# Performance work log

Measured on AMD Instinct MI355X. Metric: run time of the kernel, lower is better.

## Reference

```python
import jax, jax.numpy as jnp
import numpy as np

B, S, D = 8, 2048, 512

def setup_inputs() -> dict:
    key = jax.random.key(0)
    ks = jax.random.split(key, 9)
    scale = 1.0 / np.sqrt(D)
    return {
        "x": jax.random.normal(ks[0], (B, S, D), dtype=jnp.float32),
        "attention_mask": jax.random.uniform(ks[1], (B, S), dtype=jnp.float32),
        "Wq": jax.random.normal(ks[2], (D, D), dtype=jnp.float32) * scale,
        "bq": jax.random.normal(ks[3], (D,), dtype=jnp.float32) * 0.01,
        "Wk": jax.random.normal(ks[4], (D, D), dtype=jnp.float32) * scale,
        "bk": jax.random.normal(ks[5], (D,), dtype=jnp.float32) * 0.01,
        "Wv": jax.random.normal(ks[6], (D, D), dtype=jnp.float32) * scale,
        "bv": jax.random.normal(ks[7], (D,), dtype=jnp.float32) * 0.01,
    }

def reference(x, attention_mask, Wq, bq, Wk, bk, Wv, bv):
    # Single-head self-attention, full O(S^2) scores as in the original.
    q = jnp.einsum('bsd,df->bsf', x, Wq) + bq  # [B,S,D]
    k = jnp.einsum('bsd,df->bsf', x, Wk) + bk
    v = jnp.einsum('bsd,df->bsf', x, Wv) + bv
    scores = jnp.einsum('bqd,bkd->bqk', q, k) / jnp.sqrt(jnp.float32(D))  # [B,S,S]
    attn = jax.nn.softmax(scores, axis=2)
    weighted = jnp.einsum('bqk,bkd->bqd', attn, v)  # [B,S,D]
    # mask applied multiplicatively to the output, per original code
    return weighted * attention_mask[:, :, None]
```

## Files before the change

kernel.cpp:

```cpp
#include <hip/hip_runtime.h>
#include <math.h>
#include <stdint.h>


typedef _Float16 f16x8 __attribute__((ext_vector_type(8)));
typedef _Float16 f16x4 __attribute__((ext_vector_type(4)));
typedef _Float16 f16x2 __attribute__((ext_vector_type(2)));
typedef float f32x4 __attribute__((ext_vector_type(4)));

__device__ __forceinline__ void async16(const _Float16* g, _Float16* l) {
    __builtin_amdgcn_global_load_lds(
        (const __attribute__((address_space(1))) unsigned int*)(uintptr_t)g,
        (__attribute__((address_space(3))) unsigned int*)(unsigned int)(uintptr_t)l,
        16, 0, 0);
}

__device__ __forceinline__ float frag_sum8(f16x8 v, float acc) {
#if __has_builtin(__builtin_amdgcn_fdot2)
    const f16x2 one2 = {(_Float16)1.f, (_Float16)1.f};
    const f16x2* p = (const f16x2*)&v;
    acc = __builtin_amdgcn_fdot2(p[0], one2, acc, false);
    acc = __builtin_amdgcn_fdot2(p[1], one2, acc, false);
    acc = __builtin_amdgcn_fdot2(p[2], one2, acc, false);
    acc = __builtin_amdgcn_fdot2(p[3], one2, acc, false);
#else
#pragma unroll
    for (int j = 0; j < 8; j++) acc += (float)v[j];
#endif
    return acc;
}

template <bool WITH_RS>
__device__ __forceinline__ void mfma_gemm_core64(
    const _Float16* __restrict__ A, int lda,
    const _Float16* __restrict__ B, int ldb,
    int K, int row0, int col0,
    _Float16* sm, f32x4 acc[4][4], float rs[4])
{
    const int tid  = threadIdx.x;
    const int lane = tid & 63;
    const int wave = tid >> 6;
    const int wm   = wave >> 1, wn = wave & 1;

    const int rc  = lane >> 3;
    const int swz = ((lane & 7) ^ rc) * 8;

    const _Float16* gA[4]; const _Float16* gB[4];
    int lA[4], lB[4];
#pragma unroll
    for (int i = 0; i < 4; i++) {
        int c = wave * 4 + i;
        gA[i] = A + (size_t)(row0 + 8 * c + rc) * lda + swz;
        gB[i] = B + (size_t)(col0 + 8 * c + rc) * ldb + swz;
        lA[i] = c * 512;
        lB[i] = 8192 + c * 512;
    }

    const int fr = lane & 15;
    const int q  = lane >> 4;
    const int fx = fr & 7;

#pragma unroll
    for (int i = 0; i < 4; i++) {
        async16(gA[i], sm + lA[i]);
        async16(gB[i], sm + lB[i]);
    }

    int cur = 0;
    for (int k0 = 0;; k0 += 64) {
        const bool more = (k0 + 64) < K;
        if (more) {
            const int nb = (cur ^ 1) * 16384;
#pragma unroll
            for (int i = 0; i < 4; i++) {
                async16(gA[i] + k0 + 64, sm + nb + lA[i]);
                async16(gB[i] + k0 + 64, sm + nb + lB[i]);
            }
            asm volatile("s_waitcnt vmcnt(8)" ::: "memory");
        } else {
            asm volatile("s_waitcnt vmcnt(0)" ::: "memory");
        }
        __builtin_amdgcn_s_barrier();
        asm volatile("" ::: "memory");

        const _Float16* As = sm + cur * 16384;
        const _Float16* Bs = As + 8192;
#pragma unroll
        for (int step = 0; step < 2; step++) {
            f16x8 af[4], bf[4];
#pragma unroll
            for (int t = 0; t < 4; t++) {
                int ra = wm * 64 + t * 16 + fr;
                int rb = wn * 64 + t * 16 + fr;
                int kc = ((step * 4 + q) ^ fx) * 8;
                af[t] = *(const f16x8*)&As[ra * 64 + kc];
                bf[t] = *(const f16x8*)&Bs[rb * 64 + kc];
            }
            if (WITH_RS) {
#pragma unroll
                for (int t = 0; t < 4; t++) rs[t] = frag_sum8(af[t], rs[t]);
            }
#pragma unroll
            for (int tm = 0; tm < 4; tm++)
#pragma unroll
                for (int tn = 0; tn < 4; tn++)
                    acc[tm][tn] = __builtin_amdgcn_mfma_f32_16x16x32_f16(
                        af[tm], bf[tn], acc[tm][tn], 0, 0, 0);
        }
        asm volatile("" ::: "memory");
        if (!more) break;
        __builtin_amdgcn_s_barrier();
        cur ^= 1;
    }
}

__global__ __launch_bounds__(256) void prep(
    const float* __restrict__ x,
    const float* __restrict__ Wq, const float* __restrict__ Wk,
    const float* __restrict__ Wv,
    _Float16* __restrict__ Xh,
    _Float16* __restrict__ WqT, _Float16* __restrict__ WkT,
    _Float16* __restrict__ WvT)
{
    const int bid = blockIdx.x;
    if (bid < 8192) {
        int i = (bid * 256 + threadIdx.x) * 4;
        float4 v = *(const float4*)(x + i);
        f16x4 h;
        h.x = (_Float16)v.x; h.y = (_Float16)v.y;
        h.z = (_Float16)v.z; h.w = (_Float16)v.w;
        *(f16x4*)&Xh[i] = h;
    } else {
        int t = bid - 8192;
        int z = t >> 10;
        const float* W = (z == 0) ? Wq : (z == 1) ? Wk : Wv;
        _Float16* Wt   = (z == 0) ? WqT : (z == 1) ? WkT : WvT;
        int idx = (t & 1023) * 256 + threadIdx.x;
        int n = idx >> 9, k = idx & 511;
        Wt[idx] = (_Float16)W[k * 512 + n];
    }
}

__global__ __launch_bounds__(256) void proj_mfma(
    const _Float16* __restrict__ Xh,
    const _Float16* __restrict__ WqT, const float* __restrict__ bq,
    const _Float16* __restrict__ WkT, const float* __restrict__ bk,
    const _Float16* __restrict__ WvT, const float* __restrict__ bv,
    _Float16* __restrict__ Qh, _Float16* __restrict__ Kh,
    _Float16* __restrict__ Vt)
{
    __shared__ __align__(16) _Float16 smem[4 * 128 * 64];

    const int z = blockIdx.z;
    f32x4 acc[4][4];
#pragma unroll
    for (int i = 0; i < 4; i++)
#pragma unroll
        for (int j = 0; j < 4; j++) acc[i][j] = (f32x4){0.f, 0.f, 0.f, 0.f};
    float rs_unused[4];

    const int lane = threadIdx.x & 63, wave = threadIdx.x >> 6;
    const int wm = wave >> 1, wn = wave & 1;
    const int er = (lane >> 4) * 4, ec = lane & 15;

    if (z < 2) {
        const _Float16* Wt = (z == 0) ? WqT : WkT;
        const float* bias  = (z == 0) ? bq : bk;
        _Float16* P        = (z == 0) ? Qh : Kh;
        const float sc     = (z == 0) ? 0.04419417382415922f : 1.0f;
        const int row0 = blockIdx.x * 128, col0 = blockIdx.y * 128;
        mfma_gemm_core64<false>(Xh, 512, Wt, 512, 512, row0, col0, smem, acc,
                                rs_unused);
#pragma unroll
        for (int tm = 0; tm < 4; tm++)
#pragma unroll
            for (int tn = 0; tn < 4; tn++) {
                int col = col0 + wn * 64 + tn * 16 + ec;
                float bb = bias[col];
#pragma unroll
                for (int r = 0; r < 4; r++) {
                    int row = row0 + wm * 64 + tm * 16 + er + r;
                    P[(size_t)row * 512 + col] = (_Float16)((acc[tm][tn][r] + bb) * sc);
                }
            }
    } else {
        const int row0 = blockIdx.y * 128;
        const int col0 = blockIdx.x * 128;
        mfma_gemm_core64<false>(WvT, 512, Xh, 512, 512, row0, col0, smem, acc,
                                rs_unused);
#pragma unroll
        for (int tm = 0; tm < 4; tm++)
#pragma unroll
            for (int tn = 0; tn < 4; tn++) {
                int col = col0 + wn * 64 + tn * 16 + ec;
                size_t obase = (size_t)(col >> 11) * (512 * 2048) + (col & 2047);
#pragma unroll
                for (int r = 0; r < 4; r++) {
                    int row = row0 + wm * 64 + tm * 16 + er + r;
                    Vt[obase + (size_t)row * 2048] = (_Float16)(acc[tm][tn][r] + bv[row]);
                }
            }
    }
}

__global__ __launch_bounds__(256) void scores_mfma(
    const _Float16* __restrict__ Qh, const _Float16* __restrict__ Kh,
    _Float16* __restrict__ Sh)
{
    __shared__ __align__(16) _Float16 smem[4 * 128 * 64];
    const int bid = blockIdx.x;
    const int b   = bid & 7;
    const int rem = bid >> 3;
    const int col0 = (rem & 15) * 128;
    const int row0 = (rem >> 4) * 128;

    const _Float16* A = Qh + (size_t)b * 2048 * 512;
    const _Float16* B = Kh + (size_t)b * 2048 * 512;
    _Float16* S = Sh + (size_t)b * 2048 * 2048;

    f32x4 acc[4][4];
#pragma unroll
    for (int i = 0; i < 4; i++)
#pragma unroll
        for (int j = 0; j < 4; j++) acc[i][j] = (f32x4){0.f, 0.f, 0.f, 0.f};
    float rs_unused[4];

    mfma_gemm_core64<false>(A, 512, B, 512, 512, row0, col0, smem, acc,
                            rs_unused);

    const int lane = threadIdx.x & 63, wave = threadIdx.x >> 6;
    const int wm = wave >> 1, wn = wave & 1;
    const int er = (lane >> 4) * 4, ec = lane & 15;
#pragma unroll
    for (int tm = 0; tm < 4; tm++)
#pragma unroll
        for (int tn = 0; tn < 4; tn++) {
            int col = col0 + wn * 64 + tn * 16 + ec;
#pragma unroll
            for (int r = 0; r < 4; r++) {
                int row = row0 + wm * 64 + tm * 16 + er + r;
                S[(size_t)row * 2048 + col] = (_Float16)__expf(acc[tm][tn][r]);
            }
        }
}

__global__ __launch_bounds__(256) void av_mfma(
    const _Float16* __restrict__ Sh, const _Float16* __restrict__ Vt,
    const float* __restrict__ mask, float* __restrict__ out)
{
    __shared__ __align__(16) _Float16 smem[4 * 128 * 64];
    const int bid = blockIdx.x;
    const int b   = bid & 7;
    const int rem = bid >> 3;
    const int col0 = (rem & 3) * 128;
    const int row0 = (rem >> 2) * 128;

    const _Float16* A = Sh + (size_t)b * 2048 * 2048;
    const _Float16* B = Vt + (size_t)b * 512 * 2048;
    float* O = out + (size_t)b * 2048 * 512;
    const float* mk = mask + (size_t)b * 2048;

    f32x4 acc[4][4];
#pragma unroll
    for (int i = 0; i < 4; i++)
#pragma unroll
        for (int j = 0; j < 4; j++) acc[i][j] = (f32x4){0.f, 0.f, 0.f, 0.f};
    float rs[4] = {0.f, 0.f, 0.f, 0.f};

    mfma_gemm_core64<true>(A, 2048, B, 2048, 2048, row0, col0, smem, acc, rs);

    const int lane = threadIdx.x & 63, wave = threadIdx.x >> 6;
    const int wm = wave >> 1, wn = wave & 1;
    const int er = (lane >> 4) * 4, ec = lane & 15;

#pragma unroll
    for (int t = 0; t < 4; t++) {
        rs[t] += __shfl_xor(rs[t], 16, 64);
        rs[t] += __shfl_xor(rs[t], 32, 64);
    }
    __syncthreads();
    float* l_s = (float*)smem;
    if (wn == 0 && lane < 16) {
#pragma unroll
        for (int t = 0; t < 4; t++) l_s[wm * 64 + t * 16 + lane] = rs[t];
    }
    __syncthreads();

#pragma unroll
    for (int tm = 0; tm < 4; tm++)
#pragma unroll
        for (int r = 0; r < 4; r++) {
            int lrow = wm * 64 + tm * 16 + er + r;
            int row = row0 + lrow;
            float s = mk[row] / l_s[lrow];
#pragma unroll
            for (int tn = 0; tn < 4; tn++) {
                int col = col0 + wn * 64 + tn * 16 + ec;
                O[(size_t)row * 512 + col] = acc[tm][tn][r] * s;
            }
        }
}

extern "C" void kernel_launch(void* const* d_in, const int* in_sizes, int n_in,
                              void* d_out, int out_size, void* d_ws, size_t ws_size,
                              hipStream_t stream) {
    const float* x    = (const float*)d_in[0];
    const float* mask = (const float*)d_in[1];
    const float* Wq   = (const float*)d_in[2];
    const float* bq   = (const float*)d_in[3];
    const float* Wk   = (const float*)d_in[4];
    const float* bk   = (const float*)d_in[5];
    const float* Wv   = (const float*)d_in[6];
    const float* bv   = (const float*)d_in[7];
    float* out = (float*)d_out;

    const size_t BSD = (size_t)8 * 2048 * 512;
    _Float16* base = (_Float16*)d_ws;
    _Float16* Qh  = base;
    _Float16* Kh  = Qh + BSD;
    _Float16* Vt  = Kh + BSD;
    _Float16* WqT = Vt + BSD;
    _Float16* WkT = WqT + 512 * 512;
    _Float16* WvT = WkT + 512 * 512;
    _Float16* Xh  = WvT + 512 * 512;
    _Float16* Sh  = Xh;

    dim3 blk(256);
    prep<<<dim3(8192 + 3 * 1024), blk, 0, stream>>>(
        x, Wq, Wk, Wv, Xh, WqT, WkT, WvT);
    proj_mfma<<<dim3(128, 4, 3), blk, 0, stream>>>(
        Xh, WqT, bq, WkT, bk, WvT, bv, Qh, Kh, Vt);
    scores_mfma<<<dim3(2048), blk, 0, stream>>>(Qh, Kh, Sh);
    av_mfma<<<dim3(512), blk, 0, stream>>>(Sh, Vt, mask, out);
}
```

Before: 234.2 us.

## Switch GEMMs to 8-wave 256x128 tiles with interleaved LDS loads and MFMA

```diff
diff --git a/kernel.cpp b/kernel.cpp
--- a/kernel.cpp
+++ b/kernel.cpp
@@ -31,86 +31,156 @@
 }
 
 template <bool WITH_RS>
-__device__ __forceinline__ void mfma_gemm_core64(
-    const _Float16* __restrict__ A, int lda,
-    const _Float16* __restrict__ B, int ldb,
-    int K, int row0, int col0,
+__device__ __forceinline__ void core8(
+    const _Float16* __restrict__ A,
+    const _Float16* __restrict__ B,
+    int ld, int K, int row0, int col0,
     _Float16* sm, f32x4 acc[4][4], float rs[4])
 {
-    const int tid  = threadIdx.x;
-    const int lane = tid & 63;
-    const int wave = tid >> 6;
-    const int wm   = wave >> 1, wn = wave & 1;
-
+    constexpr int CA = 32, L = 6, BUFH = 24576;
+    const int tid = threadIdx.x, lane = tid & 63, wave = tid >> 6;
+    const int wm = wave >> 1, wn = wave & 1;
     const int rc  = lane >> 3;
     const int swz = ((lane & 7) ^ rc) * 8;
-
-    const _Float16* gA[4]; const _Float16* gB[4];
-    int lA[4], lB[4];
-#pragma unroll
-    for (int i = 0; i < 4; i++) {
-        int c = wave * 4 + i;
-        gA[i] = A + (size_t)(row0 + 8 * c + rc) * lda + swz;
-        gB[i] = B + (size_t)(col0 + 8 * c + rc) * ldb + swz;
-        lA[i] = c * 512;
-        lB[i] = 8192 + c * 512;
-    }
-
-    const int fr = lane & 15;
-    const int q  = lane >> 4;
-    const int fx = fr & 7;
-
-#pragma unroll
-    for (int i = 0; i < 4; i++) {
-        async16(gA[i], sm + lA[i]);
-        async16(gB[i], sm + lB[i]);
-    }
-
-    int cur = 0;
-    for (int k0 = 0;; k0 += 64) {
-        const bool more = (k0 + 64) < K;
-        if (more) {
-            const int nb = (cur ^ 1) * 16384;
-#pragma unroll
-            for (int i = 0; i < 4; i++) {
-                async16(gA[i] + k0 + 64, sm + nb + lA[i]);
-                async16(gB[i] + k0 + 64, sm + nb + lB[i]);
-            }
-            asm volatile("s_waitcnt vmcnt(8)" ::: "memory");
-        } else {
-            asm volatile("s_waitcnt vmcnt(0)" ::: "memory");
-        }
+    const int fr = lane & 15, q = lane >> 4, fx = fr & 7;
+
+    const _Float16* g[L];
+    int coff[L];
+#pragma unroll
+    for (int i = 0; i < L; i++) {
+        int c = wave * L + i;
+        const _Float16* base = (c < CA) ? A : B;
+        int rr = (c < CA) ? (row0 + 8 * c) : (col0 + 8 * (c - CA));
+        g[i]    = base + (size_t)(rr + rc) * ld + swz;
+        coff[i] = c * 512;
+    }
+
+    const int NT = K >> 6;
+#pragma unroll
+    for (int i = 0; i < L; i++) async16(g[i], sm + coff[i]);
+#pragma unroll
+    for (int i = 0; i < L; i++) async16(g[i] + 64, sm + BUFH + coff[i]);
+#pragma unroll
+    for (int i = 0; i < L; i++) g[i] += 128;
+    asm volatile("s_waitcnt vmcnt(6)" ::: "memory");
+    asm volatile("" ::: "memory");
+    __builtin_amdgcn_s_barrier();
+    asm volatile("" ::: "memory");
+
+#pragma unroll 2
+    for (int t = 0; t < NT; ++t) {
+        const _Float16* As = sm + (t & 1) * BUFH;
+        const _Float16* Bs = As + CA * 512;
+        f16x8 ah[2][2], b0[2][2], b1[2][2];
+
+#pragma unroll
+        for (int m = 0; m < 2; m++)
+#pragma unroll
+            for (int s = 0; s < 2; s++) {
+                int ra = (wm * 4 + m) * 16 + fr;
+                int kc = ((s * 4 + q) ^ fx) * 8;
+                ah[m][s] = *(const f16x8*)&As[ra * 64 + kc];
+            }
+#pragma unroll
+        for (int n = 0; n < 2; n++)
+#pragma unroll
+            for (int s = 0; s < 2; s++) {
+                int rb = (wn * 4 + n) * 16 + fr;
+                int kc = ((s * 4 + q) ^ fx) * 8;
+                b0[n][s] = *(const f16x8*)&Bs[rb * 64 + kc];
+            }
+        if (WITH_RS) {
+#pragma unroll
+            for (int m = 0; m < 2; m++)
+#pragma unroll
+                for (int s = 0; s < 2; s++) rs[m] = frag_sum8(ah[m][s], rs[m]);
+        }
+        __builtin_amdgcn_s_setprio(1);
+#pragma unroll
+        for (int m = 0; m < 2; m++)
+#pragma unroll
+            for (int n = 0; n < 2; n++)
+#pragma unroll
+                for (int s = 0; s < 2; s++)
+                    acc[m][n] = __builtin_amdgcn_mfma_f32_16x16x32_f16(
+                        ah[m][s], b0[n][s], acc[m][n], 0, 0, 0);
+        __builtin_amdgcn_s_setprio(0);
+
+#pragma unroll
+        for (int n = 0; n < 2; n++)
+#pragma unroll
+            for (int s = 0; s < 2; s++) {
+                int rb = (wn * 4 + 2 + n) * 16 + fr;
+                int kc = ((s * 4 + q) ^ fx) * 8;
+                b1[n][s] = *(const f16x8*)&Bs[rb * 64 + kc];
+            }
+        __builtin_amdgcn_s_setprio(1);
+#pragma unroll
+        for (int m = 0; m < 2; m++)
+#pragma unroll
+            for (int n = 0; n < 2; n++)
+#pragma unroll
+                for (int s = 0; s < 2; s++)
+                    acc[m][2 + n] = __builtin_amdgcn_mfma_f32_16x16x32_f16(
+                        ah[m][s], b1[n][s], acc[m][2 + n], 0, 0, 0);
+        __builtin_amdgcn_s_setprio(0);
+
+#pragma unroll
+        for (int m = 0; m < 2; m++)
+#pragma unroll
+            for (int s = 0; s < 2; s++) {
+                int ra = (wm * 4 + 2 + m) * 16 + fr;
+                int kc = ((s * 4 + q) ^ fx) * 8;
+                ah[m][s] = *(const f16x8*)&As[ra * 64 + kc];
+            }
+        if (WITH_RS) {
+#pragma unroll
+            for (int m = 0; m < 2; m++)
+#pragma unroll
+                for (int s = 0; s < 2; s++) rs[2 + m] = frag_sum8(ah[m][s], rs[2 + m]);
+        }
+        __builtin_amdgcn_s_setprio(1);
+#pragma unroll
+        for (int m = 0; m < 2; m++)
+#pragma unroll
+            for (int n = 0; n < 2; n++)
+#pragma unroll
+                for (int s = 0; s < 2; s++)
+                    acc[2 + m][2 + n] = __builtin_amdgcn_mfma_f32_16x16x32_f16(
+                        ah[m][s], b1[n][s], acc[2 + m][2 + n], 0, 0, 0);
+        __builtin_amdgcn_s_setprio(0);
+
+        asm volatile("s_waitcnt lgkmcnt(0)" ::: "memory");
+        asm volatile("" ::: "memory");
         __builtin_amdgcn_s_barrier();
         asm volatile("" ::: "memory");
-
-        const _Float16* As = sm + cur * 16384;
-        const _Float16* Bs = As + 8192;
-#pragma unroll
-        for (int step = 0; step < 2; step++) {
-            f16x8 af[4], bf[4];
-#pragma unroll
-            for (int t = 0; t < 4; t++) {
-                int ra = wm * 64 + t * 16 + fr;
-                int rb = wn * 64 + t * 16 + fr;
-                int kc = ((step * 4 + q) ^ fx) * 8;
-                af[t] = *(const f16x8*)&As[ra * 64 + kc];
-                bf[t] = *(const f16x8*)&Bs[rb * 64 + kc];
-            }
-            if (WITH_RS) {
-#pragma unroll
-                for (int t = 0; t < 4; t++) rs[t] = frag_sum8(af[t], rs[t]);
-            }
-#pragma unroll
-            for (int tm = 0; tm < 4; tm++)
-#pragma unroll
-                for (int tn = 0; tn < 4; tn++)
-                    acc[tm][tn] = __builtin_amdgcn_mfma_f32_16x16x32_f16(
-                        af[tm], bf[tn], acc[tm][tn], 0, 0, 0);
-        }
-        asm volatile("" ::: "memory");
-        if (!more) break;
-        __builtin_amdgcn_s_barrier();
-        cur ^= 1;
+        if (t + 2 < NT) {
+            _Float16* db = sm + (t & 1) * BUFH;
+#pragma unroll
+            for (int i = 0; i < L; i++) async16(g[i], db + coff[i]);
+#pragma unroll
+            for (int i = 0; i < L; i++) g[i] += 64;
+        }
+        __builtin_amdgcn_s_setprio(1);
+#pragma unroll
+        for (int m = 0; m < 2; m++)
+#pragma unroll
+            for (int n = 0; n < 2; n++)
+#pragma unroll
+                for (int s = 0; s < 2; s++)
+                    acc[2 + m][n] = __builtin_amdgcn_mfma_f32_16x16x32_f16(
+                        ah[m][s], b0[n][s], acc[2 + m][n], 0, 0, 0);
+        __builtin_amdgcn_s_setprio(0);
+        if (t + 2 < NT) {
+            asm volatile("s_waitcnt vmcnt(6)" ::: "memory");
+        } else if (t + 1 < NT) {
+            asm volatile("s_waitcnt vmcnt(0)" ::: "memory");
+        }
+        if (t + 1 < NT) {
+            asm volatile("" ::: "memory");
+            __builtin_amdgcn_s_barrier();
+            asm volatile("" ::: "memory");
+        }
     }
 }
 
@@ -141,7 +211,7 @@
     }
 }
 
-__global__ __launch_bounds__(256) void proj_mfma(
+__global__ __launch_bounds__(512, 2) void proj_mfma(
     const _Float16* __restrict__ Xh,
     const _Float16* __restrict__ WqT, const float* __restrict__ bq,
     const _Float16* __restrict__ WkT, const float* __restrict__ bk,
@@ -149,7 +219,7 @@
     _Float16* __restrict__ Qh, _Float16* __restrict__ Kh,
     _Float16* __restrict__ Vt)
 {
-    __shared__ __align__(16) _Float16 smem[4 * 128 * 64];
+    __shared__ __align__(16) _Float16 smem[2 * 24576];
 
     const int z = blockIdx.z;
     f32x4 acc[4][4];
@@ -168,51 +238,50 @@
         const float* bias  = (z == 0) ? bq : bk;
         _Float16* P        = (z == 0) ? Qh : Kh;
         const float sc     = (z == 0) ? 0.04419417382415922f : 1.0f;
-        const int row0 = blockIdx.x * 128, col0 = blockIdx.y * 128;
-        mfma_gemm_core64<false>(Xh, 512, Wt, 512, 512, row0, col0, smem, acc,
-                                rs_unused);
-#pragma unroll
-        for (int tm = 0; tm < 4; tm++)
-#pragma unroll
-            for (int tn = 0; tn < 4; tn++) {
-                int col = col0 + wn * 64 + tn * 16 + ec;
+        const int row0 = blockIdx.x * 256, col0 = blockIdx.y * 128;
+        core8<false>(Xh, Wt, 512, 512, row0, col0, smem, acc, rs_unused);
+#pragma unroll
+        for (int mf = 0; mf < 4; mf++)
+#pragma unroll
+            for (int nf = 0; nf < 4; nf++) {
+                int col = col0 + (wn * 4 + nf) * 16 + ec;
                 float bb = bias[col];
 #pragma unroll
                 for (int r = 0; r < 4; r++) {
-                    int row = row0 + wm * 64 + tm * 16 + er + r;
-                    P[(size_t)row * 512 + col] = (_Float16)((acc[tm][tn][r] + bb) * sc);
+                    int row = row0 + (wm * 4 + mf) * 16 + er + r;
+                    P[(size_t)row * 512 + col] = (_Float16)((acc[mf][nf][r] + bb) * sc);
                 }
             }
     } else {
-        const int row0 = blockIdx.y * 128;
-        const int col0 = blockIdx.x * 128;
-        mfma_gemm_core64<false>(WvT, 512, Xh, 512, 512, row0, col0, smem, acc,
-                                rs_unused);
-#pragma unroll
-        for (int tm = 0; tm < 4; tm++)
-#pragma unroll
-            for (int tn = 0; tn < 4; tn++) {
-                int col = col0 + wn * 64 + tn * 16 + ec;
+        const int idx = blockIdx.y * 64 + blockIdx.x;
+        const int row0 = (idx >> 7) * 256;
+        const int col0 = (idx & 127) * 128;
+        core8<false>(WvT, Xh, 512, 512, row0, col0, smem, acc, rs_unused);
+#pragma unroll
+        for (int mf = 0; mf < 4; mf++)
+#pragma unroll
+            for (int nf = 0; nf < 4; nf++) {
+                int col = col0 + (wn * 4 + nf) * 16 + ec;
                 size_t obase = (size_t)(col >> 11) * (512 * 2048) + (col & 2047);
 #pragma unroll
                 for (int r = 0; r < 4; r++) {
-                    int row = row0 + wm * 64 + tm * 16 + er + r;
-                    Vt[obase + (size_t)row * 2048] = (_Float16)(acc[tm][tn][r] + bv[row]);
+                    int row = row0 + (wm * 4 + mf) * 16 + er + r;
+                    Vt[obase + (size_t)row * 2048] = (_Float16)(acc[mf][nf][r] + bv[row]);
                 }
             }
     }
 }
 
-__global__ __launch_bounds__(256) void scores_mfma(
+__global__ __launch_bounds__(512, 2) void scores_mfma(
     const _Float16* __restrict__ Qh, const _Float16* __restrict__ Kh,
     _Float16* __restrict__ Sh)
 {
-    __shared__ __align__(16) _Float16 smem[4 * 128 * 64];
+    __shared__ __align__(16) _Float16 smem[2 * 24576];
     const int bid = blockIdx.x;
     const int b   = bid & 7;
     const int rem = bid >> 3;
     const int col0 = (rem & 15) * 128;
-    const int row0 = (rem >> 4) * 128;
+    const int row0 = (rem >> 4) * 256;
 
     const _Float16* A = Qh + (size_t)b * 2048 * 512;
     const _Float16* B = Kh + (size_t)b * 2048 * 512;
@@ -225,35 +294,34 @@
         for (int j = 0; j < 4; j++) acc[i][j] = (f32x4){0.f, 0.f, 0.f, 0.f};
     float rs_unused[4];
 
-    mfma_gemm_core64<false>(A, 512, B, 512, 512, row0, col0, smem, acc,
-                            rs_unused);
+    core8<false>(A, B, 512, 512, row0, col0, smem, acc, rs_unused);
 
     const int lane = threadIdx.x & 63, wave = threadIdx.x >> 6;
     const int wm = wave >> 1, wn = wave & 1;
     const int er = (lane >> 4) * 4, ec = lane & 15;
 #pragma unroll
-    for (int tm = 0; tm < 4; tm++)
-#pragma unroll
-        for (int tn = 0; tn < 4; tn++) {
-            int col = col0 + wn * 64 + tn * 16 + ec;
+    for (int mf = 0; mf < 4; mf++)
+#pragma unroll
+        for (int nf = 0; nf < 4; nf++) {
+            int col = col0 + (wn * 4 + nf) * 16 + ec;
 #pragma unroll
             for (int r = 0; r < 4; r++) {
-                int row = row0 + wm * 64 + tm * 16 + er + r;
-                S[(size_t)row * 2048 + col] = (_Float16)__expf(acc[tm][tn][r]);
-            }
-        }
-}
-
-__global__ __launch_bounds__(256) void av_mfma(
+                int row = row0 + (wm * 4 + mf) * 16 + er + r;
+                S[(size_t)row * 2048 + col] = (_Float16)__expf(acc[mf][nf][r]);
+            }
+        }
+}
+
+__global__ __launch_bounds__(512, 2) void av_mfma(
     const _Float16* __restrict__ Sh, const _Float16* __restrict__ Vt,
     const float* __restrict__ mask, float* __restrict__ out)
 {
-    __shared__ __align__(16) _Float16 smem[4 * 128 * 64];
+    __shared__ __align__(16) _Float16 smem[2 * 24576];
     const int bid = blockIdx.x;
     const int b   = bid & 7;
     const int rem = bid >> 3;
     const int col0 = (rem & 3) * 128;
-    const int row0 = (rem >> 2) * 128;
+    const int row0 = (rem >> 2) * 256;
 
     const _Float16* A = Sh + (size_t)b * 2048 * 2048;
     const _Float16* B = Vt + (size_t)b * 512 * 2048;
@@ -267,36 +335,36 @@
         for (int j = 0; j < 4; j++) acc[i][j] = (f32x4){0.f, 0.f, 0.f, 0.f};
     float rs[4] = {0.f, 0.f, 0.f, 0.f};
 
-    mfma_gemm_core64<true>(A, 2048, B, 2048, 2048, row0, col0, smem, acc, rs);
+    core8<true>(A, B, 2048, 2048, row0, col0, smem, acc, rs);
 
     const int lane = threadIdx.x & 63, wave = threadIdx.x >> 6;
     const int wm = wave >> 1, wn = wave & 1;
     const int er = (lane >> 4) * 4, ec = lane & 15;
 
 #pragma unroll
-    for (int t = 0; t < 4; t++) {
-        rs[t] += __shfl_xor(rs[t], 16, 64);
-        rs[t] += __shfl_xor(rs[t], 32, 64);
+    for (int mf = 0; mf < 4; mf++) {
+        rs[mf] += __shfl_xor(rs[mf], 16, 64);
+        rs[mf] += __shfl_xor(rs[mf], 32, 64);
     }
     __syncthreads();
     float* l_s = (float*)smem;
     if (wn == 0 && lane < 16) {
 #pragma unroll
-        for (int t = 0; t < 4; t++) l_s[wm * 64 + t * 16 + lane] = rs[t];
+        for (int mf = 0; mf < 4; mf++) l_s[wm * 64 + mf * 16 + lane] = rs[mf];
     }
     __syncthreads();
 
 #pragma unroll
-    for (int tm = 0; tm < 4; tm++)
+    for (int mf = 0; mf < 4; mf++)
 #pragma unroll
         for (int r = 0; r < 4; r++) {
-            int lrow = wm * 64 + tm * 16 + er + r;
+            int lrow = wm * 64 + mf * 16 + er + r;
             int row = row0 + lrow;
             float s = mk[row] / l_s[lrow];
 #pragma unroll
-            for (int tn = 0; tn < 4; tn++) {
-                int col = col0 + wn * 64 + tn * 16 + ec;
-                O[(size_t)row * 512 + col] = acc[tm][tn][r] * s;
+            for (int nf = 0; nf < 4; nf++) {
+                int col = col0 + (wn * 4 + nf) * 16 + ec;
+                O[(size_t)row * 512 + col] = acc[mf][nf][r] * s;
             }
         }
 }
@@ -325,11 +393,10 @@
     _Float16* Xh  = WvT + 512 * 512;
     _Float16* Sh  = Xh;
 
-    dim3 blk(256);
-    prep<<<dim3(8192 + 3 * 1024), blk, 0, stream>>>(
+    prep<<<dim3(8192 + 3 * 1024), dim3(256), 0, stream>>>(
         x, Wq, Wk, Wv, Xh, WqT, WkT, WvT);
-    proj_mfma<<<dim3(128, 4, 3), blk, 0, stream>>>(
+    proj_mfma<<<dim3(64, 4, 3), dim3(512), 0, stream>>>(
         Xh, WqT, bq, WkT, bk, WvT, bv, Qh, Kh, Vt);
-    scores_mfma<<<dim3(2048), blk, 0, stream>>>(Qh, Kh, Sh);
-    av_mfma<<<dim3(512), blk, 0, stream>>>(Sh, Vt, mask, out);
-}
+    scores_mfma<<<dim3(1024), dim3(512), 0, stream>>>(Qh, Kh, Sh);
+    av_mfma<<<dim3(256), dim3(512), 0, stream>>>(Sh, Vt, mask, out);
+}
```

Result: faster. 217.2 us (-7.3%).

## Restructure MFMA GEMM core into split-phase pipelined loop with staggered B loads

Applied to the files above, without the earlier changes.

```diff
diff --git a/kernel.cpp b/kernel.cpp
--- a/kernel.cpp
+++ b/kernel.cpp
@@ -30,87 +30,127 @@
     return acc;
 }
 
-template <bool WITH_RS>
-__device__ __forceinline__ void mfma_gemm_core64(
-    const _Float16* __restrict__ A, int lda,
-    const _Float16* __restrict__ B, int ldb,
-    int K, int row0, int col0,
-    _Float16* sm, f32x4 acc[4][4], float rs[4])
-{
-    const int tid  = threadIdx.x;
-    const int lane = tid & 63;
-    const int wave = tid >> 6;
-    const int wm   = wave >> 1, wn = wave & 1;
-
-    const int rc  = lane >> 3;
+#define MFMA16(a, b, c) __builtin_amdgcn_mfma_f32_16x16x32_f16(a, b, c, 0, 0, 0)
+#define BAR() __builtin_amdgcn_s_barrier()
+#define LGKM0() asm volatile("s_waitcnt lgkmcnt(0)" ::: "memory")
+
+template <int NT, bool WITH_RS>
+__device__ __forceinline__ void core128sq(
+    const _Float16* __restrict__ A, const _Float16* __restrict__ B,
+    int ld, int row0, int col0, _Float16* sm, f32x4 acc[4][4], float rs[4])
+{
+    const int tid = threadIdx.x, lane = tid & 63, wave = tid >> 6;
+    const int wm = wave >> 1, wn = wave & 1;
+    const int rc = lane >> 3;
     const int swz = ((lane & 7) ^ rc) * 8;
-
-    const _Float16* gA[4]; const _Float16* gB[4];
-    int lA[4], lB[4];
+    const int fr = lane & 15, q = lane >> 4, fx = fr & 7;
+    const size_t laneoff = (size_t)rc * ld + swz;
+
+    const _Float16* gA[4]; int lA[4];
 #pragma unroll
     for (int i = 0; i < 4; i++) {
         int c = wave * 4 + i;
-        gA[i] = A + (size_t)(row0 + 8 * c + rc) * lda + swz;
-        gB[i] = B + (size_t)(col0 + 8 * c + rc) * ldb + swz;
+        gA[i] = A + (size_t)(row0 + 8 * c) * ld + laneoff;
         lA[i] = c * 512;
-        lB[i] = 8192 + c * 512;
-    }
-
-    const int fr = lane & 15;
-    const int q  = lane >> 4;
-    const int fx = fr & 7;
-
-#pragma unroll
-    for (int i = 0; i < 4; i++) {
-        async16(gA[i], sm + lA[i]);
-        async16(gB[i], sm + lB[i]);
-    }
-
-    int cur = 0;
-    for (int k0 = 0;; k0 += 64) {
-        const bool more = (k0 + 64) < K;
-        if (more) {
-            const int nb = (cur ^ 1) * 16384;
-#pragma unroll
-            for (int i = 0; i < 4; i++) {
-                async16(gA[i] + k0 + 64, sm + nb + lA[i]);
-                async16(gB[i] + k0 + 64, sm + nb + lB[i]);
-            }
-            asm volatile("s_waitcnt vmcnt(8)" ::: "memory");
+    }
+    const _Float16* gBe[2]; const _Float16* gBl[2]; int lBe[2], lBl[2];
+#pragma unroll
+    for (int i = 0; i < 2; i++) {
+        int idx = wave * 2 + i;
+        int je = (idx & 3) + (idx >> 2) * 8;
+        int jl = je + 4;
+        gBe[i] = B + (size_t)(col0 + 8 * je) * ld + laneoff;
+        gBl[i] = B + (size_t)(col0 + 8 * jl) * ld + laneoff;
+        lBe[i] = 8192 + je * 512;
+        lBl[i] = 8192 + jl * 512;
+    }
+
+#pragma unroll
+    for (int i = 0; i < 4; i++) async16(gA[i], sm + lA[i]);
+#pragma unroll
+    for (int i = 0; i < 2; i++) async16(gBe[i], sm + lBe[i]);
+#pragma unroll
+    for (int i = 0; i < 2; i++) async16(gBl[i], sm + lBl[i]);
+#pragma unroll
+    for (int i = 0; i < 4; i++) async16(gA[i] + 64, sm + 16384 + lA[i]);
+#pragma unroll
+    for (int i = 0; i < 2; i++) async16(gBe[i] + 64, sm + 16384 + lBe[i]);
+    asm volatile("s_waitcnt vmcnt(6)" ::: "memory");
+    BAR();
+
+#pragma unroll 2
+    for (int t = 0; t < NT; ++t) {
+        const _Float16* As = sm + (t & 1) * 16384;
+        const _Float16* Bs = As + 8192;
+        f16x8 af[4][2], b0f[2][2], b1f[2][2];
+
+#pragma unroll
+        for (int m = 0; m < 4; m++)
+#pragma unroll
+            for (int s = 0; s < 2; s++) {
+                int ra = wm * 64 + m * 16 + fr;
+                af[m][s] = *(const f16x8*)&As[ra * 64 + (((s * 4 + q) ^ fx) * 8)];
+            }
+#pragma unroll
+        for (int n = 0; n < 2; n++)
+#pragma unroll
+            for (int s = 0; s < 2; s++) {
+                int rb = wn * 64 + n * 16 + fr;
+                b0f[n][s] = *(const f16x8*)&Bs[rb * 64 + (((s * 4 + q) ^ fx) * 8)];
+            }
+        if (t + 1 < NT) {
+            _Float16* nb = sm + ((t + 1) & 1) * 16384;
+#pragma unroll
+            for (int i = 0; i < 2; i++)
+                async16(gBl[i] + (t + 1) * 64, nb + lBl[i]);
+        }
+        BAR(); LGKM0();
+        if (WITH_RS) {
+#pragma unroll
+            for (int m = 0; m < 4; m++)
+#pragma unroll
+                for (int s = 0; s < 2; s++) rs[m] = frag_sum8(af[m][s], rs[m]);
+        }
+        __builtin_amdgcn_s_setprio(1);
+#pragma unroll
+        for (int s = 0; s < 2; s++)
+#pragma unroll
+            for (int m = 0; m < 4; m++)
+#pragma unroll
+                for (int n = 0; n < 2; n++)
+                    acc[m][n] = MFMA16(af[m][s], b0f[n][s], acc[m][n]);
+        __builtin_amdgcn_s_setprio(0);
+        BAR();
+
+#pragma unroll
+        for (int n = 0; n < 2; n++)
+#pragma unroll
+            for (int s = 0; s < 2; s++) {
+                int rb = wn * 64 + (2 + n) * 16 + fr;
+                b1f[n][s] = *(const f16x8*)&Bs[rb * 64 + (((s * 4 + q) ^ fx) * 8)];
+            }
+        if (t + 2 < NT) {
+            _Float16* stg = sm + (t & 1) * 16384;
+            const int k2 = (t + 2) * 64;
+#pragma unroll
+            for (int i = 0; i < 4; i++) async16(gA[i] + k2, stg + lA[i]);
+#pragma unroll
+            for (int i = 0; i < 2; i++) async16(gBe[i] + k2, stg + lBe[i]);
+            asm volatile("s_waitcnt vmcnt(6)" ::: "memory");
         } else {
             asm volatile("s_waitcnt vmcnt(0)" ::: "memory");
         }
-        __builtin_amdgcn_s_barrier();
-        asm volatile("" ::: "memory");
-
-        const _Float16* As = sm + cur * 16384;
-        const _Float16* Bs = As + 8192;
-#pragma unroll
-        for (int step = 0; step < 2; step++) {
-            f16x8 af[4], bf[4];
-#pragma unroll
-            for (int t = 0; t < 4; t++) {
-                int ra = wm * 64 + t * 16 + fr;
-                int rb = wn * 64 + t * 16 + fr;
-                int kc = ((step * 4 + q) ^ fx) * 8;
-                af[t] = *(const f16x8*)&As[ra * 64 + kc];
-                bf[t] = *(const f16x8*)&Bs[rb * 64 + kc];
-            }
-            if (WITH_RS) {
-#pragma unroll
-                for (int t = 0; t < 4; t++) rs[t] = frag_sum8(af[t], rs[t]);
-            }
-#pragma unroll
-            for (int tm = 0; tm < 4; tm++)
-#pragma unroll
-                for (int tn = 0; tn < 4; tn++)
-                    acc[tm][tn] = __builtin_amdgcn_mfma_f32_16x16x32_f16(
-                        af[tm], bf[tn], acc[tm][tn], 0, 0, 0);
-        }
-        asm volatile("" ::: "memory");
-        if (!more) break;
-        __builtin_amdgcn_s_barrier();
-        cur ^= 1;
+        BAR(); LGKM0();
+        __builtin_amdgcn_s_setprio(1);
+#pragma unroll
+        for (int s = 0; s < 2; s++)
+#pragma unroll
+            for (int m = 0; m < 4; m++)
+#pragma unroll
+                for (int n = 0; n < 2; n++)
+                    acc[m][2 + n] = MFMA16(af[m][s], b1f[n][s], acc[m][2 + n]);
+        __builtin_amdgcn_s_setprio(0);
+        BAR();
     }
 }
 
@@ -141,7 +181,7 @@
     }
 }
 
-__global__ __launch_bounds__(256) void proj_mfma(
+__global__ __launch_bounds__(256, 2) void proj_mfma(
     const _Float16* __restrict__ Xh,
     const _Float16* __restrict__ WqT, const float* __restrict__ bq,
     const _Float16* __restrict__ WkT, const float* __restrict__ bk,
@@ -149,8 +189,7 @@
     _Float16* __restrict__ Qh, _Float16* __restrict__ Kh,
     _Float16* __restrict__ Vt)
 {
-    __shared__ __align__(16) _Float16 smem[4 * 128 * 64];
-
+    __shared__ __align__(16) _Float16 smem[2 * 16384];
     const int z = blockIdx.z;
     f32x4 acc[4][4];
 #pragma unroll
@@ -169,8 +208,7 @@
         _Float16* P        = (z == 0) ? Qh : Kh;
         const float sc     = (z == 0) ? 0.04419417382415922f : 1.0f;
         const int row0 = blockIdx.x * 128, col0 = blockIdx.y * 128;
-        mfma_gemm_core64<false>(Xh, 512, Wt, 512, 512, row0, col0, smem, acc,
-                                rs_unused);
+        core128sq<8, false>(Xh, Wt, 512, row0, col0, smem, acc, rs_unused);
 #pragma unroll
         for (int tm = 0; tm < 4; tm++)
 #pragma unroll
@@ -186,8 +224,7 @@
     } else {
         const int row0 = blockIdx.y * 128;
         const int col0 = blockIdx.x * 128;
-        mfma_gemm_core64<false>(WvT, 512, Xh, 512, 512, row0, col0, smem, acc,
-                                rs_unused);
+        core128sq<8, false>(WvT, Xh, 512, row0, col0, smem, acc, rs_unused);
 #pragma unroll
         for (int tm = 0; tm < 4; tm++)
 #pragma unroll
@@ -203,11 +240,11 @@
     }
 }
 
-__global__ __launch_bounds__(256) void scores_mfma(
+__global__ __launch_bounds__(256, 2) void scores_mfma(
     const _Float16* __restrict__ Qh, const _Float16* __restrict__ Kh,
     _Float16* __restrict__ Sh)
 {
-    __shared__ __align__(16) _Float16 smem[4 * 128 * 64];
+    __shared__ __align__(16) _Float16 smem[2 * 16384];
     const int bid = blockIdx.x;
     const int b   = bid & 7;
     const int rem = bid >> 3;
@@ -225,8 +262,7 @@
         for (int j = 0; j < 4; j++) acc[i][j] = (f32x4){0.f, 0.f, 0.f, 0.f};
     float rs_unused[4];
 
-    mfma_gemm_core64<false>(A, 512, B, 512, 512, row0, col0, smem, acc,
-                            rs_unused);
+    core128sq<8, false>(A, B, 512, row0, col0, smem, acc, rs_unused);
 
     const int lane = threadIdx.x & 63, wave = threadIdx.x >> 6;
     const int wm = wave >> 1, wn = wave & 1;
@@ -244,11 +280,11 @@
         }
 }
 
-__global__ __launch_bounds__(256) void av_mfma(
+__global__ __launch_bounds__(256, 2) void av_mfma(
     const _Float16* __restrict__ Sh, const _Float16* __restrict__ Vt,
     const float* __restrict__ mask, float* __restrict__ out)
 {
-    __shared__ __align__(16) _Float16 smem[4 * 128 * 64];
+    __shared__ __align__(16) _Float16 smem[2 * 16384];
     const int bid = blockIdx.x;
     const int b   = bid & 7;
     const int rem = bid >> 3;
@@ -267,22 +303,22 @@
         for (int j = 0; j < 4; j++) acc[i][j] = (f32x4){0.f, 0.f, 0.f, 0.f};
     float rs[4] = {0.f, 0.f, 0.f, 0.f};
 
-    mfma_gemm_core64<true>(A, 2048, B, 2048, 2048, row0, col0, smem, acc, rs);
+    core128sq<32, true>(A, B, 2048, row0, col0, smem, acc, rs);
 
     const int lane = threadIdx.x & 63, wave = threadIdx.x >> 6;
     const int wm = wave >> 1, wn = wave & 1;
     const int er = (lane >> 4) * 4, ec = lane & 15;
 
 #pragma unroll
-    for (int t = 0; t < 4; t++) {
-        rs[t] += __shfl_xor(rs[t], 16, 64);
-        rs[t] += __shfl_xor(rs[t], 32, 64);
+    for (int tm = 0; tm < 4; tm++) {
+        rs[tm] += __shfl_xor(rs[tm], 16, 64);
+        rs[tm] += __shfl_xor(rs[tm], 32, 64);
     }
     __syncthreads();
     float* l_s = (float*)smem;
     if (wn == 0 && lane < 16) {
 #pragma unroll
-        for (int t = 0; t < 4; t++) l_s[wm * 64 + t * 16 + lane] = rs[t];
+        for (int tm = 0; tm < 4; tm++) l_s[wm * 64 + tm * 16 + lane] = rs[tm];
     }
     __syncthreads();
 
@@ -325,11 +361,10 @@
     _Float16* Xh  = WvT + 512 * 512;
     _Float16* Sh  = Xh;
 
-    dim3 blk(256);
-    prep<<<dim3(8192 + 3 * 1024), blk, 0, stream>>>(
+    prep<<<dim3(8192 + 3 * 1024), dim3(256), 0, stream>>>(
         x, Wq, Wk, Wv, Xh, WqT, WkT, WvT);
-    proj_mfma<<<dim3(128, 4, 3), blk, 0, stream>>>(
+    proj_mfma<<<dim3(128, 4, 3), dim3(256), 0, stream>>>(
         Xh, WqT, bq, WkT, bk, WvT, bv, Qh, Kh, Vt);
-    scores_mfma<<<dim3(2048), blk, 0, stream>>>(Qh, Kh, Sh);
-    av_mfma<<<dim3(512), blk, 0, stream>>>(Sh, Vt, mask, out);
-}
+    scores_mfma<<<dim3(2048), dim3(256), 0, stream>>>(Qh, Kh, Sh);
+    av_mfma<<<dim3(512), dim3(256), 0, stream>>>(Sh, Vt, mask, out);
+}
```

Measured after the change: 210.9 us. -9.9%, faster.
